# Kernel optimization log

Hardware: AMD Instinct MI355X
Metric: run time of the kernel (lower is better)

Reference implementation:

```python
import jax, jax.numpy as jnp
import numpy as np

B, S, D, H = 8, 2048, 768, 12

def setup_inputs() -> dict:
    key = jax.random.key(0)
    kx, km, kk, kq, kv = jax.random.split(key, 5)
    return {
        "x": jax.random.normal(kx, (B, S, D), dtype=jnp.float32),
        "mask": jax.random.randint(km, (B, 1, S), 0, 2, dtype=jnp.int32),
        "key_weight": jax.random.normal(kk, (D, H), dtype=jnp.float32),
        "query_weight": jax.random.normal(kq, (D, H), dtype=jnp.float32),
        "value_weight": jax.random.normal(kv, (D, H), dtype=jnp.float32),
    }

def reference(x, mask, key_weight, query_weight, value_weight):
    scale = 1.0 / (key_weight.shape[-1] ** 0.5)
    k = jnp.einsum('bsd,dh->bsh', x, key_weight)
    q = jnp.einsum('bsd,dh->bsh', x, query_weight)
    v = jnp.einsum('bsd,dh->bsh', x, value_weight)
    # scores: (B, S, T) — full score matrix as in the original
    scores = jnp.einsum('bsh,bth->bst', q, k) * scale
    scores = jnp.where(mask == 0, -jnp.inf, scores)
    attn = jax.nn.softmax(scores, axis=-1)
    return jnp.einsum('bst,bth->bsh', attn, v)
```

## Files before the change

kernel.cpp:

```cpp
#include <hip/hip_runtime.h>
#include <math.h>

#define QSCALE (0.2886751345948129f * 1.4426950408889634f)

#if __has_builtin(__builtin_amdgcn_exp2f)
#define EXP2F(x) __builtin_amdgcn_exp2f(x)
#else
#define EXP2F(x) exp2f(x)
#endif

typedef __attribute__((ext_vector_type(8))) _Float16 half8;
typedef __attribute__((ext_vector_type(4))) _Float16 half4_t;
typedef __attribute__((ext_vector_type(4))) float floatx4;

#define MFMA32F16(a, b, c) __builtin_amdgcn_mfma_f32_16x16x32_f16((a), (b), (c), 0, 0, 0)
#define MFMA16F16(a, b, c) __builtin_amdgcn_mfma_f32_16x16x16f16((a), (b), (c), 0, 0, 0)

static __device__ inline float bperm(float v, int addr_bytes) {
    return __int_as_float(__builtin_amdgcn_ds_bpermute(addr_bytes, __float_as_int(v)));
}

__global__ __launch_bounds__(256)
void prep(const float* __restrict__ Wq, const float* __restrict__ Wk,
          const float* __restrict__ Wv, _Float16* __restrict__ wfh,
          _Float16* __restrict__ wfl)
{
    int t = blockIdx.x * 256 + threadIdx.x;
    if (t >= 4608) return;
    int lane = t & 63;
    int nt   = (t >> 6) % 3;
    int ks   = t / 192;
    const float* W = (nt == 0) ? Wq : (nt == 1) ? Wk : Wv;
    const float scale = (nt == 0) ? QSCALE : 1.0f;
    int col = lane & 15;
    int kq  = lane >> 4;
    half8 hi, lo;
    #pragma unroll
    for (int j = 0; j < 8; ++j) {
        int dim = ks * 32 + kq * 8 + j;
        float f = (col < 12) ? W[dim * 12 + col] * scale : 0.0f;
        _Float16 h = (_Float16)f;
        hi[j] = h;
        lo[j] = (_Float16)(f - (float)h);
    }
    size_t off = ((size_t)(ks * 3 + nt) * 64 + lane) * 8;
    *(half8*)(wfh + off) = hi;
    *(half8*)(wfl + off) = lo;
}

__global__ __launch_bounds__(256, 3)
void qkv_mfma(const float* __restrict__ x, const _Float16* __restrict__ wfh,
              const _Float16* __restrict__ wfl, const int* __restrict__ mask,
              _Float16* __restrict__ qfh, _Float16* __restrict__ qfl,
              _Float16* __restrict__ kfh, _Float16* __restrict__ kfl,
              _Float16* __restrict__ vtf)
{
    __shared__ __align__(16) float smem[3072];
    const int tid  = threadIdx.x;
    const int lane = tid & 63;
    const int w    = tid >> 6;
    const int g    = ((blockIdx.x & 7) << 7) | (blockIdx.x >> 3);
    const int rowbase = g * 16;
    const int m15 = lane & 15;
    const int q8  = lane >> 4;

    const float* xbase = x + (size_t)(rowbase + m15) * 768 + q8 * 8;
    const half8* WH = (const half8*)wfh;
    const half8* WL = (const half8*)wfl;

    float xv[6][8];
    #pragma unroll
    for (int s = 0; s < 6; ++s) {
        const int ks = w * 6 + s;
        *(float4*)(xv[s])     = *(const float4*)(xbase + ks * 32);
        *(float4*)(xv[s] + 4) = *(const float4*)(xbase + ks * 32 + 4);
    }

    floatx4 acc0 = {0.f, 0.f, 0.f, 0.f};
    floatx4 acc1 = acc0, acc2 = acc0;

    half8 bh[2][3], bl[2][3];
    {
        const int ks = w * 6;
        #pragma unroll
        for (int n = 0; n < 3; ++n) {
            bh[0][n] = WH[(ks * 3 + n) * 64 + lane];
            bl[0][n] = WL[(ks * 3 + n) * 64 + lane];
        }
    }

    #pragma unroll
    for (int s = 0; s < 6; ++s) {
        const int cur = s & 1, nxt = cur ^ 1;
        if (s < 5) {
            const int ksn = w * 6 + s + 1;
            #pragma unroll
            for (int n = 0; n < 3; ++n) {
                bh[nxt][n] = WH[(ksn * 3 + n) * 64 + lane];
                bl[nxt][n] = WL[(ksn * 3 + n) * 64 + lane];
            }
        }
        half8 ah, al;
        #pragma unroll
        for (int j = 0; j < 8; ++j) {
            _Float16 h = (_Float16)xv[s][j];
            ah[j] = h;
            al[j] = (_Float16)(xv[s][j] - (float)h);
        }
        acc0 = MFMA32F16(ah, bh[cur][0], acc0);
        acc1 = MFMA32F16(ah, bh[cur][1], acc1);
        acc2 = MFMA32F16(ah, bh[cur][2], acc2);
        acc0 = MFMA32F16(al, bh[cur][0], acc0);
        acc1 = MFMA32F16(al, bh[cur][1], acc1);
        acc2 = MFMA32F16(al, bh[cur][2], acc2);
        acc0 = MFMA32F16(ah, bl[cur][0], acc0);
        acc1 = MFMA32F16(ah, bl[cur][1], acc1);
        acc2 = MFMA32F16(ah, bl[cur][2], acc2);
    }

    *(floatx4*)(smem + ((w * 3 + 0) * 64 + lane) * 4) = acc0;
    *(floatx4*)(smem + ((w * 3 + 1) * 64 + lane) * 4) = acc1;
    *(floatx4*)(smem + ((w * 3 + 2) * 64 + lane) * 4) = acc2;
    __syncthreads();
    floatx4 tot = {0.f, 0.f, 0.f, 0.f};
    if (w < 3) {
        floatx4 t0 = *(const floatx4*)(smem + ((0 * 3 + w) * 64 + lane) * 4);
        floatx4 t1 = *(const floatx4*)(smem + ((1 * 3 + w) * 64 + lane) * 4);
        floatx4 t2 = *(const floatx4*)(smem + ((2 * 3 + w) * 64 + lane) * 4);
        floatx4 t3 = *(const floatx4*)(smem + ((3 * 3 + w) * 64 + lane) * 4);
        tot = t0 + t1 + t2 + t3;
    }
    __syncthreads();

    _Float16* sh = (_Float16*)smem;
    {
        unsigned* zp = (unsigned*)smem;
        for (int i = tid; i < 1152; i += 256) zp[i] = 0u;
    }
    __syncthreads();

    if (w < 3) {
        const int col = m15;
        const int r0  = q8 * 4;
        int msk[4];
        #pragma unroll
        for (int r = 0; r < 4; ++r) msk[r] = mask[rowbase + r0 + r];
        #pragma unroll
        for (int r = 0; r < 4; ++r) {
            const int row = r0 + r;
            const float val = tot[r];
            if (w == 0) {
                if (col < 12) {
                    int idx = ((col >> 3) * 16 + row) * 8 + (col & 7);
                    _Float16 h = (_Float16)val;
                    sh[idx]       = h;
                    sh[512 + idx] = (_Float16)(val - (float)h);
                }
            } else if (w == 1) {
                if (col < 12 && msk[r]) {
                    int idx = ((col >> 3) * 16 + row) * 8 + (col & 7);
                    _Float16 h = (_Float16)val;
                    sh[1024 + idx] = h;
                    sh[1536 + idx] = (_Float16)(val - (float)h);
                }
            } else {
                if (col < 12) {
                    if (msk[r]) {
                        int idx = ((row >> 2) * 16 + col) * 4 + (row & 3);
                        sh[2048 + idx] = (_Float16)val;
                    }
                } else if (col == 12) {
                    int idx = ((row >> 2) * 16 + 12) * 4 + (row & 3);
                    sh[2048 + idx] = (_Float16)(msk[r] ? 1.f : 0.f);
                }
            }
        }
    }
    __syncthreads();

    const int bb = g >> 7;
    const int tt = g & 127;
    const size_t tb64 = (size_t)(bb * 128 + tt) * 64;
    if (w == 0) {
        ((half8*)qfh)[(size_t)g * 64 + lane] = ((const half8*)(sh))[lane];
        ((half8*)qfl)[(size_t)g * 64 + lane] = ((const half8*)(sh + 512))[lane];
    } else if (w == 1) {
        ((half8*)kfh)[tb64 + lane] = ((const half8*)(sh + 1024))[lane];
        ((half8*)kfl)[tb64 + lane] = ((const half8*)(sh + 1536))[lane];
    } else if (w == 2) {
        ((half4_t*)vtf)[tb64 + lane] = ((const half4_t*)(sh + 2048))[lane];
    }
}

__global__ __launch_bounds__(512)
void attn(const _Float16* __restrict__ qfh, const _Float16* __restrict__ qfl,
          const _Float16* __restrict__ kfh, const _Float16* __restrict__ kfl,
          const _Float16* __restrict__ vtf, float* __restrict__ out)
{
    __shared__ float cm[2048];
    __shared__ __align__(16) floatx4 co[2048];
    const int tid  = threadIdx.x;
    const int lane = tid & 63;
    const int w    = tid >> 6;
    const int bb   = blockIdx.x & 7;
    const int gl   = blockIdx.x >> 3;
    const int g0   = bb * 128 + gl * 4;
    const int m15  = lane & 15;

    half8 qh[4], ql[4];
    #pragma unroll
    for (int gi = 0; gi < 4; ++gi) {
        qh[gi] = *(const half8*)(qfh + ((size_t)(g0 + gi) * 64 + lane) * 8);
        ql[gi] = *(const half8*)(qfl + ((size_t)(g0 + gi) * 64 + lane) * 8);
    }

    const half8* KH = (const half8*)kfh + (size_t)bb * 128 * 64;
    const half8* KL = (const half8*)kfl + (size_t)bb * 128 * 64;
    const half4_t* VT = (const half4_t*)vtf + (size_t)bb * 128 * 64;

    const int a16 = (lane ^ 16) << 2;
    const int a32 = (lane ^ 32) << 2;
    const int a48 = (lane ^ 48) << 2;

    float m[4] = {-INFINITY, -INFINITY, -INFINITY, -INFINITY};
    floatx4 o[4];
    #pragma unroll
    for (int gi = 0; gi < 4; ++gi) o[gi] = (floatx4){0.f, 0.f, 0.f, 0.f};

    int t = w;
    half8 kh = KH[t * 64 + lane];
    half8 kl = KL[t * 64 + lane];
    half4_t va = VT[t * 64 + lane];
    for (; t < 128; t += 8) {
        half8 nkh, nkl; half4_t nva;
        if (t + 8 < 128) {
            nkh = KH[(t + 8) * 64 + lane];
            nkl = KL[(t + 8) * 64 + lane];
            nva = VT[(t + 8) * 64 + lane];
        }
        floatx4 s[4];
        #pragma unroll
        for (int gi = 0; gi < 4; ++gi) s[gi] = (floatx4){0.f, 0.f, 0.f, 0.f};
        #pragma unroll
        for (int gi = 0; gi < 4; ++gi) s[gi] = MFMA32F16(kh, qh[gi], s[gi]);
        #pragma unroll
        for (int gi = 0; gi < 4; ++gi) s[gi] = MFMA32F16(kl, qh[gi], s[gi]);
        #pragma unroll
        for (int gi = 0; gi < 4; ++gi) s[gi] = MFMA32F16(kh, ql[gi], s[gi]);
        #pragma unroll
        for (int gi = 0; gi < 4; ++gi) {
            float pm = fmaxf(fmaxf(s[gi].x, s[gi].y), fmaxf(s[gi].z, s[gi].w));
            float b1 = bperm(pm, a16);
            float b2 = bperm(pm, a32);
            float b3 = bperm(pm, a48);
            pm = fmaxf(fmaxf(pm, b1), fmaxf(b2, b3));
            float mnew = fmaxf(m[gi], pm);
            float corr = EXP2F(m[gi] - mnew);
            o[gi].x *= corr; o[gi].y *= corr; o[gi].z *= corr; o[gi].w *= corr;
            half4_t pb;
            pb[0] = (_Float16)EXP2F(s[gi].x - mnew);
            pb[1] = (_Float16)EXP2F(s[gi].y - mnew);
            pb[2] = (_Float16)EXP2F(s[gi].z - mnew);
            pb[3] = (_Float16)EXP2F(s[gi].w - mnew);
            o[gi] = MFMA16F16(va, pb, o[gi]);
            m[gi] = mnew;
        }
        kh = nkh; kl = nkl; va = nva;
    }

    #pragma unroll
    for (int gi = 0; gi < 4; ++gi) {
        cm[(gi * 8 + w) * 64 + lane] = m[gi];
        co[(gi * 8 + w) * 64 + lane] = o[gi];
    }
    __syncthreads();
    if (w < 4) {
        const int gi = w;
        float gm = -INFINITY;
        #pragma unroll
        for (int w2 = 0; w2 < 8; ++w2) gm = fmaxf(gm, cm[(gi * 8 + w2) * 64 + lane]);
        floatx4 O = {0.f, 0.f, 0.f, 0.f};
        #pragma unroll
        for (int w2 = 0; w2 < 8; ++w2) {
            float f = EXP2F(cm[(gi * 8 + w2) * 64 + lane] - gm);
            floatx4 ow = co[(gi * 8 + w2) * 64 + lane];
            O.x += ow.x * f; O.y += ow.y * f; O.z += ow.z * f; O.w += ow.w * f;
        }
        float L = bperm(O.x, (48 + m15) << 2);
        float inv = 1.0f / L;
        if ((lane >> 4) < 3) {
            float4 ov = make_float4(O.x * inv, O.y * inv, O.z * inv, O.w * inv);
            *(float4*)(out + ((size_t)(g0 + gi) * 16 + m15) * 12 + (lane >> 4) * 4) = ov;
        }
    }
}

extern "C" void kernel_launch(void* const* d_in, const int* in_sizes, int n_in,
                              void* d_out, int out_size, void* d_ws, size_t ws_size,
                              hipStream_t stream) {
    const float* x    = (const float*)d_in[0];
    const int*   mask = (const int*)  d_in[1];
    const float* Wk   = (const float*)d_in[2];
    const float* Wq   = (const float*)d_in[3];
    const float* Wv   = (const float*)d_in[4];
    float* out = (float*)d_out;

    char* base = (char*)d_ws;
    _Float16* qfh = (_Float16*)(base);
    _Float16* qfl = (_Float16*)(base + (1u << 20));
    _Float16* kfh = (_Float16*)(base + (2u << 20));
    _Float16* kfl = (_Float16*)(base + (3u << 20));
    _Float16* vtf = (_Float16*)(base + (4u << 20));
    _Float16* wfh = (_Float16*)(base + 4718592);
    _Float16* wfl = (_Float16*)(base + 4718592 + 73728);

    prep<<<18, 256, 0, stream>>>(Wq, Wk, Wv, wfh, wfl);
    qkv_mfma<<<1024, 256, 0, stream>>>(x, wfh, wfl, mask, qfh, qfl, kfh, kfl, vtf);
    attn<<<256, 512, 0, stream>>>(qfh, qfl, kfh, kfl, vtf, out);
}
```

Baseline: 117.7 us.

## Pack split-fp16 K hi/lo into one K=32 operand to cut QK MFMAs

The head dimension is only 12 of the 32 MFMA K-slots, so K's hi and lo fp16 halves are packed into a single 32-wide operand. Q is duplicated to match: one operand holds [qh, qh] and the other [ql, 0]. The three QK score MFMAs per tile become two, and one K stream disappears from both global memory traffic and registers. The attention loop also switches to a two-deep register prefetch of K and V. The cost is slightly more shared-memory packing work in the QKV kernel and longer prefetch register lifetimes.

```diff
diff --git a/kernel.cpp b/kernel.cpp
--- a/kernel.cpp
+++ b/kernel.cpp
@@ -51,9 +51,8 @@
 __global__ __launch_bounds__(256, 3)
 void qkv_mfma(const float* __restrict__ x, const _Float16* __restrict__ wfh,
               const _Float16* __restrict__ wfl, const int* __restrict__ mask,
-              _Float16* __restrict__ qfh, _Float16* __restrict__ qfl,
-              _Float16* __restrict__ kfh, _Float16* __restrict__ kfl,
-              _Float16* __restrict__ vtf)
+              _Float16* __restrict__ qp1f, _Float16* __restrict__ qp2f,
+              _Float16* __restrict__ kpkf, _Float16* __restrict__ vtf)
 {
     __shared__ __align__(16) float smem[3072];
     const int tid  = threadIdx.x;
@@ -135,7 +134,7 @@
     _Float16* sh = (_Float16*)smem;
     {
         unsigned* zp = (unsigned*)smem;
-        for (int i = tid; i < 1152; i += 256) zp[i] = 0u;
+        for (int i = tid; i < 896; i += 256) zp[i] = 0u;
     }
     __syncthreads();
 
@@ -152,26 +151,29 @@
             if (w == 0) {
                 if (col < 12) {
                     int idx = ((col >> 3) * 16 + row) * 8 + (col & 7);
+                    int idx2 = (((col >> 3) + 2) * 16 + row) * 8 + (col & 7);
                     _Float16 h = (_Float16)val;
-                    sh[idx]       = h;
-                    sh[512 + idx] = (_Float16)(val - (float)h);
+                    sh[idx]        = h;
+                    sh[idx2]       = h;
+                    sh[512 + idx]  = (_Float16)(val - (float)h);
                 }
             } else if (w == 1) {
                 if (col < 12 && msk[r]) {
-                    int idx = ((col >> 3) * 16 + row) * 8 + (col & 7);
+                    int idx  = ((col >> 3) * 16 + row) * 8 + (col & 7);
+                    int idx2 = (((col >> 3) + 2) * 16 + row) * 8 + (col & 7);
                     _Float16 h = (_Float16)val;
-                    sh[1024 + idx] = h;
-                    sh[1536 + idx] = (_Float16)(val - (float)h);
+                    sh[1024 + idx]  = h;
+                    sh[1024 + idx2] = (_Float16)(val - (float)h);
                 }
             } else {
                 if (col < 12) {
                     if (msk[r]) {
                         int idx = ((row >> 2) * 16 + col) * 4 + (row & 3);
-                        sh[2048 + idx] = (_Float16)val;
+                        sh[1536 + idx] = (_Float16)val;
                     }
                 } else if (col == 12) {
                     int idx = ((row >> 2) * 16 + 12) * 4 + (row & 3);
-                    sh[2048 + idx] = (_Float16)(msk[r] ? 1.f : 0.f);
+                    sh[1536 + idx] = (_Float16)(msk[r] ? 1.f : 0.f);
                 }
             }
         }
@@ -182,20 +184,19 @@
     const int tt = g & 127;
     const size_t tb64 = (size_t)(bb * 128 + tt) * 64;
     if (w == 0) {
-        ((half8*)qfh)[(size_t)g * 64 + lane] = ((const half8*)(sh))[lane];
-        ((half8*)qfl)[(size_t)g * 64 + lane] = ((const half8*)(sh + 512))[lane];
+        ((half8*)qp1f)[(size_t)g * 64 + lane] = ((const half8*)(sh))[lane];
+        ((half8*)qp2f)[(size_t)g * 64 + lane] = ((const half8*)(sh + 512))[lane];
     } else if (w == 1) {
-        ((half8*)kfh)[tb64 + lane] = ((const half8*)(sh + 1024))[lane];
-        ((half8*)kfl)[tb64 + lane] = ((const half8*)(sh + 1536))[lane];
+        ((half8*)kpkf)[tb64 + lane] = ((const half8*)(sh + 1024))[lane];
     } else if (w == 2) {
-        ((half4_t*)vtf)[tb64 + lane] = ((const half4_t*)(sh + 2048))[lane];
+        ((half4_t*)vtf)[tb64 + lane] = ((const half4_t*)(sh + 1536))[lane];
     }
 }
 
 __global__ __launch_bounds__(512)
-void attn(const _Float16* __restrict__ qfh, const _Float16* __restrict__ qfl,
-          const _Float16* __restrict__ kfh, const _Float16* __restrict__ kfl,
-          const _Float16* __restrict__ vtf, float* __restrict__ out)
+void attn(const _Float16* __restrict__ qp1f, const _Float16* __restrict__ qp2f,
+          const _Float16* __restrict__ kpkf, const _Float16* __restrict__ vtf,
+          float* __restrict__ out)
 {
     __shared__ float cm[2048];
     __shared__ __align__(16) floatx4 co[2048];
@@ -207,15 +208,14 @@
     const int g0   = bb * 128 + gl * 4;
     const int m15  = lane & 15;
 
-    half8 qh[4], ql[4];
+    half8 qp1[4], qp2[4];
     #pragma unroll
     for (int gi = 0; gi < 4; ++gi) {
-        qh[gi] = *(const half8*)(qfh + ((size_t)(g0 + gi) * 64 + lane) * 8);
-        ql[gi] = *(const half8*)(qfl + ((size_t)(g0 + gi) * 64 + lane) * 8);
-    }
-
-    const half8* KH = (const half8*)kfh + (size_t)bb * 128 * 64;
-    const half8* KL = (const half8*)kfl + (size_t)bb * 128 * 64;
+        qp1[gi] = *(const half8*)(qp1f + ((size_t)(g0 + gi) * 64 + lane) * 8);
+        qp2[gi] = *(const half8*)(qp2f + ((size_t)(g0 + gi) * 64 + lane) * 8);
+    }
+
+    const half8* KP = (const half8*)kpkf + (size_t)bb * 128 * 64;
     const half4_t* VT = (const half4_t*)vtf + (size_t)bb * 128 * 64;
 
     const int a16 = (lane ^ 16) << 2;
@@ -227,26 +227,28 @@
     #pragma unroll
     for (int gi = 0; gi < 4; ++gi) o[gi] = (floatx4){0.f, 0.f, 0.f, 0.f};
 
-    int t = w;
-    half8 kh = KH[t * 64 + lane];
-    half8 kl = KL[t * 64 + lane];
-    half4_t va = VT[t * 64 + lane];
-    for (; t < 128; t += 8) {
-        half8 nkh, nkl; half4_t nva;
-        if (t + 8 < 128) {
-            nkh = KH[(t + 8) * 64 + lane];
-            nkl = KL[(t + 8) * 64 + lane];
-            nva = VT[(t + 8) * 64 + lane];
+    half8 kp[2];  half4_t va[2];
+    kp[0] = KP[w * 64 + lane];
+    va[0] = VT[w * 64 + lane];
+    kp[1] = KP[(w + 8) * 64 + lane];
+    va[1] = VT[(w + 8) * 64 + lane];
+
+    for (int it = 0; it < 16; ++it) {
+        const int cur = it & 1;
+        half8 ck = kp[cur];
+        half4_t cv = va[cur];
+        const int tn = w + (it + 2) * 8;
+        if (tn < 128) {
+            kp[cur] = KP[tn * 64 + lane];
+            va[cur] = VT[tn * 64 + lane];
         }
         floatx4 s[4];
         #pragma unroll
         for (int gi = 0; gi < 4; ++gi) s[gi] = (floatx4){0.f, 0.f, 0.f, 0.f};
         #pragma unroll
-        for (int gi = 0; gi < 4; ++gi) s[gi] = MFMA32F16(kh, qh[gi], s[gi]);
-        #pragma unroll
-        for (int gi = 0; gi < 4; ++gi) s[gi] = MFMA32F16(kl, qh[gi], s[gi]);
-        #pragma unroll
-        for (int gi = 0; gi < 4; ++gi) s[gi] = MFMA32F16(kh, ql[gi], s[gi]);
+        for (int gi = 0; gi < 4; ++gi) s[gi] = MFMA32F16(ck, qp1[gi], s[gi]);
+        #pragma unroll
+        for (int gi = 0; gi < 4; ++gi) s[gi] = MFMA32F16(ck, qp2[gi], s[gi]);
         #pragma unroll
         for (int gi = 0; gi < 4; ++gi) {
             float pm = fmaxf(fmaxf(s[gi].x, s[gi].y), fmaxf(s[gi].z, s[gi].w));
@@ -262,10 +264,9 @@
             pb[1] = (_Float16)EXP2F(s[gi].y - mnew);
             pb[2] = (_Float16)EXP2F(s[gi].z - mnew);
             pb[3] = (_Float16)EXP2F(s[gi].w - mnew);
-            o[gi] = MFMA16F16(va, pb, o[gi]);
+            o[gi] = MFMA16F16(cv, pb, o[gi]);
             m[gi] = mnew;
         }
-        kh = nkh; kl = nkl; va = nva;
     }
 
     #pragma unroll
@@ -306,15 +307,14 @@
     float* out = (float*)d_out;
 
     char* base = (char*)d_ws;
-    _Float16* qfh = (_Float16*)(base);
-    _Float16* qfl = (_Float16*)(base + (1u << 20));
-    _Float16* kfh = (_Float16*)(base + (2u << 20));
-    _Float16* kfl = (_Float16*)(base + (3u << 20));
-    _Float16* vtf = (_Float16*)(base + (4u << 20));
-    _Float16* wfh = (_Float16*)(base + 4718592);
-    _Float16* wfl = (_Float16*)(base + 4718592 + 73728);
+    _Float16* qp1f = (_Float16*)(base);
+    _Float16* qp2f = (_Float16*)(base + (1u << 20));
+    _Float16* kpkf = (_Float16*)(base + (2u << 20));
+    _Float16* vtf  = (_Float16*)(base + (3u << 20));
+    _Float16* wfh  = (_Float16*)(base + 3670016);
+    _Float16* wfl  = (_Float16*)(base + 3670016 + 73728);
 
     prep<<<18, 256, 0, stream>>>(Wq, Wk, Wv, wfh, wfl);
-    qkv_mfma<<<1024, 256, 0, stream>>>(x, wfh, wfl, mask, qfh, qfl, kfh, kfl, vtf);
-    attn<<<256, 512, 0, stream>>>(qfh, qfl, kfh, kfl, vtf, out);
-}
+    qkv_mfma<<<1024, 256, 0, stream>>>(x, wfh, wfl, mask, qp1f, qp2f, kpkf, vtf);
+    attn<<<256, 512, 0, stream>>>(qp1f, qp2f, kpkf, vtf, out);
+}
```

After: 173.9 us. 1.48x slower.
